# Kernel tuning notes

Hardware: AMD Instinct MI355X
Metric: run time of the kernel (lower is better)

The kernel has to match this reference:

```python
import jax, jax.numpy as jnp
import numpy as np

B, C, J, T, S = 16, 4, 19, 256, 10
D1, D2, DS, O = 64, 64, 128, 64  # embed hidden, embed out, similarity dim, out channels
EPS = 1e-5


def setup_inputs() -> dict:
    key = jax.random.key(0)
    ks = jax.random.split(key, 12)
    sc = 0.05
    return {
        'x': jax.random.normal(ks[0], (B, C, J, T, S), dtype=jnp.float32),
        'gamma': jnp.ones((C * J * T,), dtype=jnp.float32),
        'beta': jnp.zeros((C * J * T,), dtype=jnp.float32),
        'w1': jax.random.normal(ks[1], (D1, C), dtype=jnp.float32) * sc,
        'b1': jax.random.normal(ks[2], (D1,), dtype=jnp.float32) * sc,
        'w2': jax.random.normal(ks[3], (D2, D1), dtype=jnp.float32) * sc,
        'b2': jax.random.normal(ks[4], (D2,), dtype=jnp.float32) * sc,
        'ws1': jax.random.normal(ks[5], (DS, D2), dtype=jnp.float32) * sc,
        'bs1': jax.random.normal(ks[6], (DS,), dtype=jnp.float32) * sc,
        'ws2': jax.random.normal(ks[7], (DS, D2), dtype=jnp.float32) * sc,
        'bs2': jax.random.normal(ks[8], (DS,), dtype=jnp.float32) * sc,
        'W': jax.random.normal(ks[9], (D2, O), dtype=jnp.float32) * sc,
    }


def _bn(x, gamma, beta):
    # BatchNorm1d in training mode on x viewed as (B, C*J*T, S): stats over (batch, step)
    b, c, j, t, s = x.shape
    xf = x.reshape(b, c * j * t, s)
    mean = xf.mean(axis=(0, 2), keepdims=True)
    var = ((xf - mean) ** 2).mean(axis=(0, 2), keepdims=True)
    xn = (xf - mean) * jax.lax.rsqrt(var + EPS)
    xn = xn * gamma[None, :, None] + beta[None, :, None]
    return xn.reshape(b, c, j, t, s)


def _conv1x1(x, w, bias):
    # Conv3d with kernel 1 == channel mix: (B,Cin,J,T,S) x (Cout,Cin)
    y = jnp.einsum('bcjts,oc->bojts', x, w)
    return y + bias[None, :, None, None, None]


def reference(x, gamma, beta, w1, b1, w2, b2, ws1, bs1, ws2, bs2, W):
    # embed: norm -> 1x1 conv -> relu -> 1x1 conv -> relu
    h = _bn(x, gamma, beta)
    h = jax.nn.relu(_conv1x1(h, w1, b1))
    h = jax.nn.relu(_conv1x1(h, w2, b2))  # (B, 64, J, T, S)
    # compute_similarity: learned dense adjacency over joints per (b, s, t)
    s1 = _conv1x1(h, ws1, bs1)  # (B, 128, J, T, S)
    s2 = _conv1x1(h, ws2, bs2)
    logits = jnp.einsum('bcjts,bckts->bstjk', s1, s2)  # (B, S, T, J, J)
    att = jax.nn.softmax(logits, axis=-1)
    # aggregate node features then mix channels with weight (64, O)
    agg = jnp.einsum('bstjk,bckts->bstjc', att, h)  # (B, S, T, J, 64)
    out = jnp.einsum('bstjc,co->bojts', agg, W)  # (B, O, J, T, S)
    return out
```

## Files before the change

kernel.cpp:

```cpp
#include <hip/hip_runtime.h>
#include <hip/hip_bf16.h>

#define B_   16
#define C_   4
#define J_   19
#define T_   256
#define S_   10
#define JT_  4864
#define CJT_ 19456

#define WS_SCALE 0
#define WS_SHIFT 19456
#define WS_Q2    38912
#define WS_F16_BYTE ((38912 + 64) * 4)
#define H_W2 0
#define H_Q  4096
#define H_WT 8192

typedef _Float16 f16;
typedef _Float16 half8 __attribute__((ext_vector_type(8)));
typedef float f32x4 __attribute__((ext_vector_type(4)));

__device__ __forceinline__ float bf2f(__hip_bfloat16 v) { return __bfloat162float(v); }
__device__ __forceinline__ float bfbits2f(unsigned short u) {
    unsigned int w = ((unsigned int)u) << 16;
    return __builtin_bit_cast(float, w);
}
__device__ __forceinline__ float ldin(const void* p, int i, bool f32) {
    if (f32) return ((const float*)p)[i];
    return bf2f(((const __hip_bfloat16*)p)[i]);
}
__device__ __forceinline__ bool dtype_is_f32(const void* gamma) {
    return ((const unsigned short*)gamma)[0] == 0;
}
__device__ __forceinline__ f32x4 mfma16(half8 a, half8 b, f32x4 c) {
    return __builtin_amdgcn_mfma_f32_16x16x32_f16(a, b, c, 0, 0, 0);
}

extern "C" __global__ __launch_bounds__(1024)
void setup_kernel(const void* __restrict__ x, const void* __restrict__ gamma,
                  const void* __restrict__ beta, const void* __restrict__ w2,
                  const void* __restrict__ ws1, const void* __restrict__ ws2,
                  const void* __restrict__ bs1, const void* __restrict__ Wm,
                  float* __restrict__ wsf)
{
    const bool f32 = dtype_is_f32(gamma);
    const int tid = threadIdx.x;
    __shared__ float redS[4][256], redQ[4][256];

    if (blockIdx.x < 76) {
        const int cj = blockIdx.x;
        const int t  = tid & 255;
        const int bq = tid >> 8;
        float sum = 0.f, sq = 0.f;
        for (int bb = 0; bb < 4; ++bb) {
            int b = bq * 4 + bb;
            size_t base = ((size_t)(b * 76 + cj)) * 2560 + (size_t)t * 10;
            float va[10];
            if (f32) {
                __builtin_memcpy(va, (const float*)x + base, 40);
            } else {
                unsigned short ua[10];
                __builtin_memcpy(ua, (const unsigned short*)x + base, 20);
#pragma unroll
                for (int k = 0; k < 10; ++k) va[k] = bfbits2f(ua[k]);
            }
#pragma unroll
            for (int k = 0; k < 10; ++k) {
                sum += va[k];
                sq  = fmaf(va[k], va[k], sq);
            }
        }
        redS[bq][t] = sum;
        redQ[bq][t] = sq;
        __syncthreads();
        if (bq == 0) {
            sum = redS[0][t] + redS[1][t] + redS[2][t] + redS[3][t];
            sq  = redQ[0][t] + redQ[1][t] + redQ[2][t] + redQ[3][t];
            int ch = cj * 256 + t;
            float mean = sum * (1.f / 160.f);
            float var  = fmaxf(sq * (1.f / 160.f) - mean * mean, 0.f);
            float scl = ldin(gamma, ch, f32) * rsqrtf(var + 1e-5f);
            wsf[WS_SCALE + ch] = scl;
            wsf[WS_SHIFT + ch] = ldin(beta, ch, f32) - mean * scl;
        }
        return;
    }

    f16* hws = (f16*)((char*)wsf + WS_F16_BYTE);
    int id = (blockIdx.x - 76) * 1024 + tid;
    if (id < 4096) {
        int a = id >> 6, b = id & 63;
        float acc = 0.f;
        for (int ds = 0; ds < 128; ++ds)
            acc = fmaf(ldin(ws1, ds * 64 + a, f32), ldin(ws2, ds * 64 + b, f32), acc);
        hws[H_Q + id] = (f16)acc;
    } else if (id < 8192) {
        int i = id - 4096;
        hws[H_W2 + i] = (f16)ldin(w2, i, f32);
    } else if (id < 12288) {
        int i = id - 8192;
        int o = i >> 6, c = i & 63;
        hws[H_WT + i] = (f16)ldin(Wm, c * 64 + o, f32);
    } else if (id < 12352) {
        int b = id - 12288;
        float acc = 0.f;
        for (int ds = 0; ds < 128; ++ds)
            acc = fmaf(ldin(ws2, ds * 64 + b, f32), ldin(bs1, ds, f32), acc);
        wsf[WS_Q2 + b] = acc;
    }
}

#define HR 112
#define HSTR 72
#define WTSTR 168
#define ATSTR 40
#define OBSTR 72

#define A1_OFF 0
#define A2_OFF 21504
#define A3_OFF 37632
#define A4_OFF 53760
#define ARENA_BYTES 61760

extern "C" __global__ __launch_bounds__(256, 2)
void fused_kernel(const void* __restrict__ x,
                  const void* __restrict__ w1, const void* __restrict__ b1,
                  const void* __restrict__ b2, const void* __restrict__ gamma,
                  const float* __restrict__ wsf, void* __restrict__ outv)
{
    const bool f32o = dtype_is_f32(gamma);
    const int tid = threadIdx.x;
    const int lane = tid & 63;
    const int wave = tid >> 6;
    const int l15 = lane & 15;
    const int q4 = lane >> 4;

    const int hw  = blockIdx.x;
    const int bid = (hw & 7) * 1024 + (hw >> 3);
    const int b  = bid >> 9;
    const int t  = (bid >> 1) & 255;
    const int sh = bid & 1;

    __shared__ __align__(16) unsigned char arena[ARENA_BYTES];
    __shared__ __align__(16) float w1f[256];
    __shared__ float b1f[64], b2f[64], q2f[64], vbuf[112];

    f16* h1row  = (f16*)(arena + A1_OFF);
    f16* hWT    = (f16*)(arena + A1_OFF);
    f16* h2row  = (f16*)(arena + A2_OFF);
    f16* outb   = (f16*)(arena + A2_OFF);
    f16* urow   = (f16*)(arena + A3_OFF);
    f16* att    = (f16*)(arena + A3_OFF);
    float* logits = (float*)(arena + A4_OFF);
    float* xnr    = (float*)(arena + A4_OFF);

    const f16* hws = (const f16*)((const char*)wsf + WS_F16_BYTE);

    w1f[tid] = ldin(w1, tid, f32o);
    if (tid < 64) {
        b1f[tid] = ldin(b1, tid, f32o);
        b2f[tid] = ldin(b2, tid, f32o);
        q2f[tid] = wsf[WS_Q2 + tid];
    }
    for (int e = tid; e < 400; e += 256) {
        int R = e >> 2, c = e & 3;
        int sL = R / 20, j = R - sL * 20;
        float val = 0.f;
        if (j < 19) {
            int sg = sh * 5 + sL;
            int xidx = ((b * 4 + c) * 19 + j) * 2560 + t * 10 + sg;
            int ch = (c * 19 + j) * 256 + t;
            val = ldin(x, xidx, f32o) * wsf[WS_SCALE + ch] + wsf[WS_SHIFT + ch];
        }
        xnr[e] = val;
    }
    __syncthreads();

    {
        int d = tid & 63;
        float4 wr = *(const float4*)&w1f[d * 4];
        float bb = b1f[d];
        for (int r = 0; r < 25; ++r) {
            int R = wave * 25 + r;
            float4 xc = *(const float4*)&xnr[R * 4];
            float h = fmaf(xc.x, wr.x, fmaf(xc.y, wr.y, fmaf(xc.z, wr.z, fmaf(xc.w, wr.w, bb))));
            h1row[R * HSTR + d] = (f16)fmaxf(h, 0.f);
        }
    }
    __syncthreads();

#define LDFRAG(base, row0, stride, koff) \
    (*(const half8*)((base) + ((row0) + l15) * (stride) + (koff) + (q4 << 3)))

    {
        int n0 = wave * 16;
        half8 B0 = LDFRAG(hws + H_W2, n0, 64, 0);
        half8 B1 = LDFRAG(hws + H_W2, n0, 64, 32);
        float bias = b2f[n0 + l15];
        for (int m = 0; m < 7; ++m) {
            half8 A0 = LDFRAG(h1row, m * 16, HSTR, 0);
            half8 A1 = LDFRAG(h1row, m * 16, HSTR, 32);
            f32x4 c = {bias, bias, bias, bias};
            c = mfma16(A0, B0, c);
            c = mfma16(A1, B1, c);
#pragma unroll
            for (int i = 0; i < 4; ++i) {
                int r = m * 16 + q4 * 4 + i;
                h2row[r * HSTR + n0 + l15] = (f16)fmaxf(c[i], 0.f);
            }
        }
    }
    __syncthreads();

    {
        int n0 = wave * 16;
        half8 B0 = LDFRAG(hws + H_Q, n0, 64, 0);
        half8 B1 = LDFRAG(hws + H_Q, n0, 64, 32);
        for (int m = 0; m < 7; ++m) {
            half8 A0 = LDFRAG(h2row, m * 16, HSTR, 0);
            half8 A1 = LDFRAG(h2row, m * 16, HSTR, 32);
            f32x4 c = {0.f, 0.f, 0.f, 0.f};
            c = mfma16(A0, B0, c);
            c = mfma16(A1, B1, c);
#pragma unroll
            for (int i = 0; i < 4; ++i) {
                int r = m * 16 + q4 * 4 + i;
                urow[r * HSTR + n0 + l15] = (f16)c[i];
            }
        }
        if (tid < 100) {
            const f16* hr = &h2row[tid * HSTR];
            float acc = 0.f;
#pragma unroll
            for (int g = 0; g < 8; ++g) {
                half8 hv = *(const half8*)&hr[g * 8];
#pragma unroll
                for (int jj = 0; jj < 8; ++jj)
                    acc = fmaf((float)hv[jj], q2f[g * 8 + jj], acc);
            }
            vbuf[tid] = acc;
        }
    }
    __syncthreads();

    {
        for (int e = tid; e < 64 * 5 * 13; e += 256) {
            int o = e / 65, rem = e - o * 65;
            int s = rem / 13, kk = 19 + (rem - s * 13);
            hWT[o * WTSTR + s * 32 + kk] = (f16)0.f;
        }
        int n0 = wave * 16;
        half8 B0 = LDFRAG(hws + H_WT, n0, 64, 0);
        half8 B1 = LDFRAG(hws + H_WT, n0, 64, 32);
        for (int m = 0; m < 7; ++m) {
            half8 A0 = LDFRAG(h2row, m * 16, HSTR, 0);
            half8 A1 = LDFRAG(h2row, m * 16, HSTR, 32);
            f32x4 c = {0.f, 0.f, 0.f, 0.f};
            c = mfma16(A0, B0, c);
            c = mfma16(A1, B1, c);
#pragma unroll
            for (int i = 0; i < 4; ++i) {
                int r = m * 16 + q4 * 4 + i;
                int s = r / 20, j = r - s * 20;
                if (r < 100 && j < 19)
                    hWT[(n0 + l15) * WTSTR + s * 32 + j] = (f16)c[i];
            }
        }
        for (int task = wave; task < 10; task += 4) {
            int s = task >> 1, nt = task & 1;
            int n0g = s * 20 + nt * 16;
            half8 Bb0 = LDFRAG(urow, n0g, HSTR, 0);
            half8 Bb1 = LDFRAG(urow, n0g, HSTR, 32);
            int kloc = nt * 16 + l15;
            bool kval = kloc < 19;
            float vv = vbuf[s * 20 + ((kloc < 19) ? kloc : 0)];
#pragma unroll
            for (int mt = 0; mt < 2; ++mt) {
                int m0 = s * 20 + mt * 16;
                half8 A0 = LDFRAG(h2row, m0, HSTR, 0);
                half8 A1 = LDFRAG(h2row, m0, HSTR, 32);
                f32x4 c = {0.f, 0.f, 0.f, 0.f};
                c = mfma16(A0, Bb0, c);
                c = mfma16(A1, Bb1, c);
#pragma unroll
                for (int i = 0; i < 4; ++i) {
                    int j = mt * 16 + q4 * 4 + i;
                    if (j < 19 && kval)
                        logits[s * 400 + j * 20 + kloc] = c[i] + vv;
                }
            }
        }
    }
    __syncthreads();

    if (tid < 95) {
        int sL = tid / 19, j = tid - sL * 19;
        int R = sL * 20 + j;
        const float4* lp = (const float4*)&logits[sL * 400 + j * 20];
        float4 e0 = lp[0], e1 = lp[1], e2 = lp[2], e3 = lp[3], e4 = lp[4];
        e4.w = -1e30f;
        float m = e0.x;
        m = fmaxf(m, e0.y); m = fmaxf(m, e0.z); m = fmaxf(m, e0.w);
        m = fmaxf(m, e1.x); m = fmaxf(m, e1.y); m = fmaxf(m, e1.z); m = fmaxf(m, e1.w);
        m = fmaxf(m, e2.x); m = fmaxf(m, e2.y); m = fmaxf(m, e2.z); m = fmaxf(m, e2.w);
        m = fmaxf(m, e3.x); m = fmaxf(m, e3.y); m = fmaxf(m, e3.z); m = fmaxf(m, e3.w);
        m = fmaxf(m, e4.x); m = fmaxf(m, e4.y); m = fmaxf(m, e4.z);
        e0.x = __expf(e0.x - m); e0.y = __expf(e0.y - m); e0.z = __expf(e0.z - m); e0.w = __expf(e0.w - m);
        e1.x = __expf(e1.x - m); e1.y = __expf(e1.y - m); e1.z = __expf(e1.z - m); e1.w = __expf(e1.w - m);
        e2.x = __expf(e2.x - m); e2.y = __expf(e2.y - m); e2.z = __expf(e2.z - m); e2.w = __expf(e2.w - m);
        e3.x = __expf(e3.x - m); e3.y = __expf(e3.y - m); e3.z = __expf(e3.z - m); e3.w = __expf(e3.w - m);
        e4.x = __expf(e4.x - m); e4.y = __expf(e4.y - m); e4.z = __expf(e4.z - m);
        float sum = e0.x + e0.y + e0.z + e0.w + e1.x + e1.y + e1.z + e1.w
                  + e2.x + e2.y + e2.z + e2.w + e3.x + e3.y + e3.z + e3.w
                  + e4.x + e4.y + e4.z;
        float rs = 1.f / sum;
        half8 h0 = {(f16)(e0.x * rs), (f16)(e0.y * rs), (f16)(e0.z * rs), (f16)(e0.w * rs),
                    (f16)(e1.x * rs), (f16)(e1.y * rs), (f16)(e1.z * rs), (f16)(e1.w * rs)};
        half8 h1 = {(f16)(e2.x * rs), (f16)(e2.y * rs), (f16)(e2.z * rs), (f16)(e2.w * rs),
                    (f16)(e3.x * rs), (f16)(e3.y * rs), (f16)(e3.z * rs), (f16)(e3.w * rs)};
        half8 h2v = {(f16)(e4.x * rs), (f16)(e4.y * rs), (f16)(e4.z * rs),
                     (f16)0.f, (f16)0.f, (f16)0.f, (f16)0.f, (f16)0.f};
        half8 h3v = {(f16)0.f, (f16)0.f, (f16)0.f, (f16)0.f,
                     (f16)0.f, (f16)0.f, (f16)0.f, (f16)0.f};
        f16* ap = &att[R * ATSTR];
        *(half8*)(ap + 0)  = h0;
        *(half8*)(ap + 8)  = h1;
        *(half8*)(ap + 16) = h2v;
        *(half8*)(ap + 24) = h3v;
    }
    __syncthreads();

    for (int task = wave; task < 20; task += 4) {
        int s = task >> 2, nt = task & 3;
        int o0 = nt * 16;
        half8 Bf = *(const half8*)&hWT[(o0 + l15) * WTSTR + s * 32 + (q4 << 3)];
#pragma unroll
        for (int mt = 0; mt < 2; ++mt) {
            int m0 = s * 20 + mt * 16;
            half8 Af = *(const half8*)&att[(m0 + l15) * ATSTR + (q4 << 3)];
            f32x4 c = {0.f, 0.f, 0.f, 0.f};
            c = mfma16(Af, Bf, c);
#pragma unroll
            for (int i = 0; i < 4; ++i) {
                int j = mt * 16 + q4 * 4 + i;
                if (j < 19)
                    outb[(s * 19 + j) * OBSTR + o0 + l15] = (f16)c[i];
            }
        }
    }
    __syncthreads();

    for (int p = 0; p < 5; ++p) {
        int id = p * 256 + tid;
        if (id < 1216) {
            int o = id / 19, j = id - o * 19;
            int obase = ((b * 64 + o) * 19 + j) * 2560 + t * 10 + sh * 5;
            if (f32o) {
                float tmp[5];
#pragma unroll
                for (int sl = 0; sl < 5; ++sl)
                    tmp[sl] = (float)outb[(sl * 19 + j) * OBSTR + o];
                __builtin_memcpy((float*)outv + obase, tmp, 20);
            } else {
                unsigned short tmp[5];
#pragma unroll
                for (int sl = 0; sl < 5; ++sl) {
                    __hip_bfloat16 h = __float2bfloat16((float)outb[(sl * 19 + j) * OBSTR + o]);
                    tmp[sl] = __builtin_bit_cast(unsigned short, h);
                }
                __builtin_memcpy((__hip_bfloat16*)outv + obase, tmp, 10);
            }
        }
    }
}

extern "C" void kernel_launch(void* const* d_in, const int* in_sizes, int n_in,
                              void* d_out, int out_size, void* d_ws, size_t ws_size,
                              hipStream_t stream)
{
    const void* x     = d_in[0];
    const void* gamma = d_in[1];
    const void* beta  = d_in[2];
    const void* w1    = d_in[3];
    const void* b1    = d_in[4];
    const void* w2    = d_in[5];
    const void* b2    = d_in[6];
    const void* ws1   = d_in[7];
    const void* bs1   = d_in[8];
    const void* ws2   = d_in[9];
    const void* bs2   = d_in[10];
    const void* Wm    = d_in[11];
    float* wsf = (float*)d_ws;

    hipLaunchKernelGGL(setup_kernel, dim3(89), dim3(1024), 0, stream,
                       x, gamma, beta, w2, ws1, ws2, bs1, Wm, wsf);
    hipLaunchKernelGGL(fused_kernel, dim3(B_ * T_ * 2), dim3(256), 0, stream,
                       x, w1, b1, b2, gamma, wsf, d_out);
}
```

Baseline: 436.6 us.

## Shrink LDS footprint with swizzled rows and fp16 logits for three blocks per CU

Replaces the padded 72-stride h1/h2/u row buffers with unpadded 64-wide XOR-swizzled layouts, stores logits and the bias vector in fp16, and packs the small weight and bias arrays into the shared arena. This cuts shared memory per block from about 63KB to about 54KB, and launch bounds are raised to allow 3 blocks per CU for more latency hiding. Storing logits in fp16 costs some softmax precision, and the tighter register budget could cause spills.

Measured after the change: 439.9 us. About the same (+0.8%).

```diff
diff --git a/kernel.cpp b/kernel.cpp
--- a/kernel.cpp
+++ b/kernel.cpp
@@ -19,6 +19,7 @@
 
 typedef _Float16 f16;
 typedef _Float16 half8 __attribute__((ext_vector_type(8)));
+typedef _Float16 f16x4 __attribute__((ext_vector_type(4)));
 typedef float f32x4 __attribute__((ext_vector_type(4)));
 
 __device__ __forceinline__ float bf2f(__hip_bfloat16 v) { return __bfloat162float(v); }
@@ -35,6 +36,9 @@
 }
 __device__ __forceinline__ f32x4 mfma16(half8 a, half8 b, f32x4 c) {
     return __builtin_amdgcn_mfma_f32_16x16x32_f16(a, b, c, 0, 0, 0);
+}
+__device__ __forceinline__ int swz64(int row, int col) {
+    return (row << 6) + ((((col >> 3) ^ (row & 7)) << 3)) + (col & 7);
 }
 
 extern "C" __global__ __launch_bounds__(1024)
@@ -111,19 +115,23 @@
     }
 }
 
-#define HR 112
-#define HSTR 72
 #define WTSTR 168
 #define ATSTR 40
 #define OBSTR 72
 
 #define A1_OFF 0
 #define A2_OFF 21504
-#define A3_OFF 37632
-#define A4_OFF 53760
-#define ARENA_BYTES 61760
-
-extern "C" __global__ __launch_bounds__(256, 2)
+#define A3_OFF 35840
+#define A4_OFF 50176
+#define XNR_OFF 50176
+#define W1F_OFF 51776
+#define B1F_OFF 52800
+#define B2F_OFF 53056
+#define Q2F_OFF 53312
+#define VBH_OFF 53976
+#define ARENA_BYTES 54176
+
+extern "C" __global__ __launch_bounds__(256, 3)
 void fused_kernel(const void* __restrict__ x,
                   const void* __restrict__ w1, const void* __restrict__ b1,
                   const void* __restrict__ b2, const void* __restrict__ gamma,
@@ -143,8 +151,6 @@
     const int sh = bid & 1;
 
     __shared__ __align__(16) unsigned char arena[ARENA_BYTES];
-    __shared__ __align__(16) float w1f[256];
-    __shared__ float b1f[64], b2f[64], q2f[64], vbuf[112];
 
     f16* h1row  = (f16*)(arena + A1_OFF);
     f16* hWT    = (f16*)(arena + A1_OFF);
@@ -152,8 +158,13 @@
     f16* outb   = (f16*)(arena + A2_OFF);
     f16* urow   = (f16*)(arena + A3_OFF);
     f16* att    = (f16*)(arena + A3_OFF);
-    float* logits = (float*)(arena + A4_OFF);
-    float* xnr    = (float*)(arena + A4_OFF);
+    f16* logits = (f16*)(arena + A4_OFF);
+    f16* vbh    = (f16*)(arena + VBH_OFF);
+    float* xnr  = (float*)(arena + XNR_OFF);
+    float* w1f  = (float*)(arena + W1F_OFF);
+    float* b1f  = (float*)(arena + B1F_OFF);
+    float* b2f  = (float*)(arena + B2F_OFF);
+    float* q2f  = (float*)(arena + Q2F_OFF);
 
     const f16* hws = (const f16*)((const char*)wsf + WS_F16_BYTE);
 
@@ -185,13 +196,16 @@
             int R = wave * 25 + r;
             float4 xc = *(const float4*)&xnr[R * 4];
             float h = fmaf(xc.x, wr.x, fmaf(xc.y, wr.y, fmaf(xc.z, wr.z, fmaf(xc.w, wr.w, bb))));
-            h1row[R * HSTR + d] = (f16)fmaxf(h, 0.f);
+            h1row[swz64(R, d)] = (f16)fmaxf(h, 0.f);
         }
     }
     __syncthreads();
 
 #define LDFRAG(base, row0, stride, koff) \
     (*(const half8*)((base) + ((row0) + l15) * (stride) + (koff) + (q4 << 3)))
+#define LDSWZ(base, row0, koff) \
+    (*(const half8*)((base) + (((row0) + l15) << 6) + \
+        ((((((koff) >> 3) + q4) ^ (((row0) + l15) & 7)) << 3))))
 
     {
         int n0 = wave * 16;
@@ -199,15 +213,15 @@
         half8 B1 = LDFRAG(hws + H_W2, n0, 64, 32);
         float bias = b2f[n0 + l15];
         for (int m = 0; m < 7; ++m) {
-            half8 A0 = LDFRAG(h1row, m * 16, HSTR, 0);
-            half8 A1 = LDFRAG(h1row, m * 16, HSTR, 32);
+            half8 A0 = LDSWZ(h1row, m * 16, 0);
+            half8 A1 = LDSWZ(h1row, m * 16, 32);
             f32x4 c = {bias, bias, bias, bias};
             c = mfma16(A0, B0, c);
             c = mfma16(A1, B1, c);
 #pragma unroll
             for (int i = 0; i < 4; ++i) {
                 int r = m * 16 + q4 * 4 + i;
-                h2row[r * HSTR + n0 + l15] = (f16)fmaxf(c[i], 0.f);
+                h2row[swz64(r, n0 + l15)] = (f16)fmaxf(c[i], 0.f);
             }
         }
     }
@@ -218,28 +232,28 @@
         half8 B0 = LDFRAG(hws + H_Q, n0, 64, 0);
         half8 B1 = LDFRAG(hws + H_Q, n0, 64, 32);
         for (int m = 0; m < 7; ++m) {
-            half8 A0 = LDFRAG(h2row, m * 16, HSTR, 0);
-            half8 A1 = LDFRAG(h2row, m * 16, HSTR, 32);
+            half8 A0 = LDSWZ(h2row, m * 16, 0);
+            half8 A1 = LDSWZ(h2row, m * 16, 32);
             f32x4 c = {0.f, 0.f, 0.f, 0.f};
             c = mfma16(A0, B0, c);
             c = mfma16(A1, B1, c);
 #pragma unroll
             for (int i = 0; i < 4; ++i) {
                 int r = m * 16 + q4 * 4 + i;
-                urow[r * HSTR + n0 + l15] = (f16)c[i];
+                urow[swz64(r, n0 + l15)] = (f16)c[i];
             }
         }
         if (tid < 100) {
-            const f16* hr = &h2row[tid * HSTR];
+            const f16* hr = &h2row[tid << 6];
             float acc = 0.f;
 #pragma unroll
             for (int g = 0; g < 8; ++g) {
-                half8 hv = *(const half8*)&hr[g * 8];
+                half8 hv = *(const half8*)&hr[(g ^ (tid & 7)) << 3];
 #pragma unroll
                 for (int jj = 0; jj < 8; ++jj)
                     acc = fmaf((float)hv[jj], q2f[g * 8 + jj], acc);
             }
-            vbuf[tid] = acc;
+            vbh[tid] = (f16)acc;
         }
     }
     __syncthreads();
@@ -254,8 +268,8 @@
         half8 B0 = LDFRAG(hws + H_WT, n0, 64, 0);
         half8 B1 = LDFRAG(hws + H_WT, n0, 64, 32);
         for (int m = 0; m < 7; ++m) {
-            half8 A0 = LDFRAG(h2row, m * 16, HSTR, 0);
-            half8 A1 = LDFRAG(h2row, m * 16, HSTR, 32);
+            half8 A0 = LDSWZ(h2row, m * 16, 0);
+            half8 A1 = LDSWZ(h2row, m * 16, 32);
             f32x4 c = {0.f, 0.f, 0.f, 0.f};
             c = mfma16(A0, B0, c);
             c = mfma16(A1, B1, c);
@@ -270,16 +284,16 @@
         for (int task = wave; task < 10; task += 4) {
             int s = task >> 1, nt = task & 1;
             int n0g = s * 20 + nt * 16;
-            half8 Bb0 = LDFRAG(urow, n0g, HSTR, 0);
-            half8 Bb1 = LDFRAG(urow, n0g, HSTR, 32);
+            half8 Bb0 = LDSWZ(urow, n0g, 0);
+            half8 Bb1 = LDSWZ(urow, n0g, 32);
             int kloc = nt * 16 + l15;
             bool kval = kloc < 19;
-            float vv = vbuf[s * 20 + ((kloc < 19) ? kloc : 0)];
+            float vv = (float)vbh[s * 20 + ((kloc < 19) ? kloc : 0)];
 #pragma unroll
             for (int mt = 0; mt < 2; ++mt) {
                 int m0 = s * 20 + mt * 16;
-                half8 A0 = LDFRAG(h2row, m0, HSTR, 0);
-                half8 A1 = LDFRAG(h2row, m0, HSTR, 32);
+                half8 A0 = LDSWZ(h2row, m0, 0);
+                half8 A1 = LDSWZ(h2row, m0, 32);
                 f32x4 c = {0.f, 0.f, 0.f, 0.f};
                 c = mfma16(A0, Bb0, c);
                 c = mfma16(A1, Bb1, c);
@@ -287,7 +301,7 @@
                 for (int i = 0; i < 4; ++i) {
                     int j = mt * 16 + q4 * 4 + i;
                     if (j < 19 && kval)
-                        logits[s * 400 + j * 20 + kloc] = c[i] + vv;
+                        logits[s * 380 + j * 20 + kloc] = (f16)(c[i] + vv);
                 }
             }
         }
@@ -297,37 +311,33 @@
     if (tid < 95) {
         int sL = tid / 19, j = tid - sL * 19;
         int R = sL * 20 + j;
-        const float4* lp = (const float4*)&logits[sL * 400 + j * 20];
-        float4 e0 = lp[0], e1 = lp[1], e2 = lp[2], e3 = lp[3], e4 = lp[4];
-        e4.w = -1e30f;
-        float m = e0.x;
-        m = fmaxf(m, e0.y); m = fmaxf(m, e0.z); m = fmaxf(m, e0.w);
-        m = fmaxf(m, e1.x); m = fmaxf(m, e1.y); m = fmaxf(m, e1.z); m = fmaxf(m, e1.w);
-        m = fmaxf(m, e2.x); m = fmaxf(m, e2.y); m = fmaxf(m, e2.z); m = fmaxf(m, e2.w);
-        m = fmaxf(m, e3.x); m = fmaxf(m, e3.y); m = fmaxf(m, e3.z); m = fmaxf(m, e3.w);
-        m = fmaxf(m, e4.x); m = fmaxf(m, e4.y); m = fmaxf(m, e4.z);
-        e0.x = __expf(e0.x - m); e0.y = __expf(e0.y - m); e0.z = __expf(e0.z - m); e0.w = __expf(e0.w - m);
-        e1.x = __expf(e1.x - m); e1.y = __expf(e1.y - m); e1.z = __expf(e1.z - m); e1.w = __expf(e1.w - m);
-        e2.x = __expf(e2.x - m); e2.y = __expf(e2.y - m); e2.z = __expf(e2.z - m); e2.w = __expf(e2.w - m);
-        e3.x = __expf(e3.x - m); e3.y = __expf(e3.y - m); e3.z = __expf(e3.z - m); e3.w = __expf(e3.w - m);
-        e4.x = __expf(e4.x - m); e4.y = __expf(e4.y - m); e4.z = __expf(e4.z - m);
-        float sum = e0.x + e0.y + e0.z + e0.w + e1.x + e1.y + e1.z + e1.w
-                  + e2.x + e2.y + e2.z + e2.w + e3.x + e3.y + e3.z + e3.w
-                  + e4.x + e4.y + e4.z;
+        const f16x4* lp4 = (const f16x4*)(logits + sL * 380 + j * 20);
+        float lv[20];
+#pragma unroll
+        for (int g = 0; g < 5; ++g) {
+            f16x4 v = lp4[g];
+#pragma unroll
+            for (int k = 0; k < 4; ++k) lv[g * 4 + k] = (float)v[k];
+        }
+        float m = lv[0];
+#pragma unroll
+        for (int k = 1; k < 19; ++k) m = fmaxf(m, lv[k]);
+        float e[19], sum = 0.f;
+#pragma unroll
+        for (int k = 0; k < 19; ++k) { e[k] = __expf(lv[k] - m); sum += e[k]; }
         float rs = 1.f / sum;
-        half8 h0 = {(f16)(e0.x * rs), (f16)(e0.y * rs), (f16)(e0.z * rs), (f16)(e0.w * rs),
-                    (f16)(e1.x * rs), (f16)(e1.y * rs), (f16)(e1.z * rs), (f16)(e1.w * rs)};
-        half8 h1 = {(f16)(e2.x * rs), (f16)(e2.y * rs), (f16)(e2.z * rs), (f16)(e2.w * rs),
-                    (f16)(e3.x * rs), (f16)(e3.y * rs), (f16)(e3.z * rs), (f16)(e3.w * rs)};
-        half8 h2v = {(f16)(e4.x * rs), (f16)(e4.y * rs), (f16)(e4.z * rs),
-                     (f16)0.f, (f16)0.f, (f16)0.f, (f16)0.f, (f16)0.f};
-        half8 h3v = {(f16)0.f, (f16)0.f, (f16)0.f, (f16)0.f,
-                     (f16)0.f, (f16)0.f, (f16)0.f, (f16)0.f};
+        half8 H[4];
+#pragma unroll
+        for (int g = 0; g < 4; ++g)
+#pragma unroll
+            for (int k = 0; k < 8; ++k) {
+                int idx = g * 8 + k;
+                H[g][k] = (idx < 19) ? (f16)(e[idx] * rs) : (f16)0.f;
+            }
         f16* ap = &att[R * ATSTR];
-        *(half8*)(ap + 0)  = h0;
-        *(half8*)(ap + 8)  = h1;
-        *(half8*)(ap + 16) = h2v;
-        *(half8*)(ap + 24) = h3v;
+#pragma unroll
+        for (int g = 0; g < 4; ++g)
+            *(half8*)(ap + g * 8) = H[g];
     }
     __syncthreads();
 
```
